# Kernel tuning notes

Hardware: AMD Instinct MI355X
Metric: run time of the kernel (lower is better)

The kernel has to match this reference:

```python
import jax, jax.numpy as jnp
import numpy as np

TREE_DEPTH = 6
IN_F, OUT_F = 1024, 1024
BATCH = 2048
N_LEAVES = 2 ** TREE_DEPTH
N_NODES = N_LEAVES - 1


def _tree_routes(depth):
    """Static routing table: for each leaf, the decision-node index visited at
    each depth and whether the leaf takes the sigmoid (1) or 1-sigmoid (0) branch.
    Mirrors the torch traversal: node = 2*node + 1 + bit; bits of leaf id LSB-first."""
    n_leaves = 2 ** depth
    idx = np.zeros((n_leaves, depth), dtype=np.int32)
    pos = np.zeros((n_leaves, depth), dtype=bool)
    for l in range(n_leaves):
        node, index = 0, l
        for d in range(depth):
            idx[l, d] = node
            pos[l, d] = (index % 2 == 0)
            node = node * 2 + 1 + index % 2
            index >>= 1
    return idx, pos

ROUTE_IDX, ROUTE_POS = _tree_routes(TREE_DEPTH)


def setup_inputs() -> dict:
    key = jax.random.key(0)
    kx, kwd, kwl = jax.random.split(key, 3)
    scale = 0.02  # keep sigmoid/softmax logits in a sane range
    x = jax.random.normal(kx, (BATCH, IN_F), dtype=jnp.float32)
    Wd = jax.random.normal(kwd, (N_NODES, IN_F), dtype=jnp.float32) * scale
    bd = jnp.zeros((N_NODES,), dtype=jnp.float32)
    Wl = jax.random.normal(kwl, (N_LEAVES, OUT_F, IN_F), dtype=jnp.float32) * scale
    bl = jnp.zeros((N_LEAVES, OUT_F), dtype=jnp.float32)
    return {"x": x, "Wd": Wd, "bd": bd, "Wl": Wl, "bl": bl}


def reference(x, Wd, bd, Wl, bl):
    # All decision node probabilities in one GEMM: [B, n_nodes]
    dprob = jax.nn.sigmoid(x @ Wd.T + bd)
    # Gather per-leaf path probs [B, L, depth] and take path product -> routing [B, L]
    path = dprob[:, ROUTE_IDX]                      # [B, L, D]
    path = jnp.where(ROUTE_POS, path, 1.0 - path)
    routing = jnp.prod(path, axis=-1)               # [B, L]
    # All leaf experts in one batched GEMM: [B, L, out], softmax over out (torch dim=1)
    leaf_logits = jnp.einsum('bi,loi->blo', x, Wl) + bl
    leaves = jax.nn.softmax(leaf_logits, axis=-1)
    # Routing-weighted sum over leaves
    return jnp.einsum('bl,blo->bo', routing, leaves)
```

## Files before the change

### kernel.cpp

```cpp
#include <hip/hip_runtime.h>
#include <hip/hip_bf16.h>

#define BATCH 2048
#define KD 1024
#define ND 1024
#define NLEAF 64
#define BM 256
#define BN 256

typedef __attribute__((ext_vector_type(8))) short bf16x8;
typedef __attribute__((ext_vector_type(4))) float f32x4;
typedef __attribute__((ext_vector_type(8))) _Float16 f16x8;

#define WLB_OFF 0ULL
#define XB_OFF  134217728ULL
#define RT_OFF  138412032ULL
#define LG_OFF  138936320ULL

__device__ __forceinline__ unsigned short f2bf(float f) {
  unsigned int u = __float_as_uint(f);
  u += 0x7fffu + ((u >> 16) & 1u);
  return (unsigned short)(u >> 16);
}

__device__ __forceinline__ void gload_lds16(const void* g, void* l) {
  __builtin_amdgcn_global_load_lds(
      (const __attribute__((address_space(1))) unsigned int*)g,
      (__attribute__((address_space(3))) unsigned int*)l, 16, 0, 0);
}

__global__ void __launch_bounds__(256) convert_kernel(
    const float* __restrict__ Wl, const float* __restrict__ x,
    unsigned short* __restrict__ wlb, unsigned short* __restrict__ xb) {
  const long long WL4 = 16777216LL;
  const long long X4  = 524288LL;
  long long i = (long long)blockIdx.x * 256 + threadIdx.x;
  const long long stride = (long long)gridDim.x * 256;
  for (; i < WL4 + X4; i += stride) {
    float4 v;
    if (i < WL4) v = ((const float4*)Wl)[i];
    else         v = ((const float4*)x)[i - WL4];
    ushort4 o;
    o.x = f2bf(v.x); o.y = f2bf(v.y); o.z = f2bf(v.z); o.w = f2bf(v.w);
    if (i < WL4) ((ushort4*)wlb)[i] = o;
    else         ((ushort4*)xb)[i - WL4] = o;
  }
}

__global__ void __launch_bounds__(256) routing_kernel(
    const float* __restrict__ x, const float* __restrict__ Wd,
    const float* __restrict__ bd, float* __restrict__ rt) {
  __shared__ float xs[4][KD];
  __shared__ float sdp[4][64];
  const int tid = threadIdx.x;
  const int b0 = blockIdx.x * 4;
  const float4* xsrc = (const float4*)(x + (size_t)b0 * KD);
  float4* xdst = (float4*)&xs[0][0];
  for (int i = tid; i < KD; i += 256) xdst[i] = xsrc[i];
  __syncthreads();
  const int wv = tid >> 6, ln = tid & 63;
  const int b = b0 + wv;
  if (ln < 63) {
    const float4* wrow = (const float4*)(Wd + (size_t)ln * KD);
    const float4* xr = (const float4*)&xs[wv][0];
    float4 a = {0.f, 0.f, 0.f, 0.f};
    for (int k = 0; k < KD / 4; ++k) {
      float4 w = wrow[k], xv = xr[k];
      a.x += w.x * xv.x; a.y += w.y * xv.y; a.z += w.z * xv.z; a.w += w.w * xv.w;
    }
    float z = a.x + a.y + a.z + a.w + bd[ln];
    sdp[wv][ln] = 1.f / (1.f + __expf(-z));
  }
  __syncthreads();
  float prod = 1.f;
  int node = 0, index = ln;
  for (int d = 0; d < 6; ++d) {
    float pv = sdp[wv][node];
    prod *= (index & 1) ? (1.f - pv) : pv;
    node = node * 2 + 1 + (index & 1);
    index >>= 1;
  }
  rt[(size_t)b * NLEAF + ln] = prod;
}

#define GBODY(CURA, CURB, NXTA, NXTB, S, VMASM, DOREAD)                      \
  {                                                                          \
    if ((S) + 3 < 32) STAGE((S) + 3);                                        \
    asm volatile(VMASM ::: "memory");                                        \
    asm volatile("s_waitcnt lgkmcnt(0)" ::: "memory");                       \
    __builtin_amdgcn_sched_barrier(0);                                       \
    asm volatile("s_barrier" ::: "memory");                                  \
    __builtin_amdgcn_s_setprio(1);                                           \
    if (DOREAD) {                                                            \
      const char* nbuf = smem + (((S) + 1) & 3) * 32768;                     \
      _Pragma("unroll")                                                      \
      for (int mi = 0; mi < 8; ++mi)                                         \
        NXTA[mi] = *(const bf16x8*)(nbuf + offA[mi]);                        \
      _Pragma("unroll")                                                      \
      for (int ni = 0; ni < 4; ++ni)                                         \
        NXTB[ni] = *(const bf16x8*)(nbuf + 16384 + offB[ni]);                \
    }                                                                        \
    _Pragma("unroll")                                                        \
    for (int mi = 0; mi < 8; ++mi)                                           \
      _Pragma("unroll")                                                      \
      for (int ni = 0; ni < 4; ++ni)                                         \
        acc[mi][ni] = __builtin_amdgcn_mfma_f32_16x16x32_bf16(               \
            CURA[mi], CURB[ni], acc[mi][ni], 0, 0, 0);                       \
    if (DOREAD) {                                                            \
      _Pragma("unroll")                                                      \
      for (int r = 0; r < 12; ++r) {                                         \
        __builtin_amdgcn_sched_group_barrier(0x100, 1, 0);    \
        __builtin_amdgcn_sched_group_barrier(0x008, 2, 0);    \
      }                                                                      \
      __builtin_amdgcn_sched_group_barrier(0x008, 8, 0);      \
    }                                                                        \
    __builtin_amdgcn_s_setprio(0);                                           \
    __builtin_amdgcn_sched_barrier(0);                                       \
  }

__global__ void __launch_bounds__(512, 2) gemm_kernel(
    const unsigned short* __restrict__ A, const unsigned short* __restrict__ B,
    const float* __restrict__ blg, _Float16* __restrict__ C, int ntile) {
  extern __shared__ char smem[];
  const int tid = threadIdx.x;
  const int w = tid >> 6, ln = tid & 63;
  const int wm = w >> 2, wn = w & 3;
  const int g = ln >> 4, r16 = ln & 15;
  const int bid = blockIdx.x;
  const int j = bid >> 3;
  const int bm = (j & 7) * BM;
  const int bn = (((j >> 3) << 3) + (bid & 7)) * BN;
  const long long ldc = (long long)ntile * 256;

  const int rS = tid >> 2;
  const int cS = tid & 3;
  const int csrc = cS ^ ((rS >> 1) & 3);
  const unsigned short* ga0 = A + (size_t)(bm + rS) * KD + csrc * 8;
  const unsigned short* ga1 = ga0 + (size_t)128 * KD;
  const unsigned short* gb0 = B + (size_t)(bn + rS) * KD + csrc * 8;
  const unsigned short* gb1 = gb0 + (size_t)128 * KD;
  const int ldsw = w * 1024;

  auto STAGE = [&](int t) {
    char* base = smem + (t & 3) * 32768;
    const size_t ko = (size_t)t * 32;
    gload_lds16(ga0 + ko, base + ldsw);
    gload_lds16(ga1 + ko, base + 8192 + ldsw);
    gload_lds16(gb0 + ko, base + 16384 + ldsw);
    gload_lds16(gb1 + ko, base + 24576 + ldsw);
  };

  int offA[8], offB[4];
#pragma unroll
  for (int mi = 0; mi < 8; ++mi) {
    const int row = wm * 128 + mi * 16 + r16;
    offA[mi] = row * 64 + (g ^ ((row >> 1) & 3)) * 16;
  }
#pragma unroll
  for (int ni = 0; ni < 4; ++ni) {
    const int row = wn * 64 + ni * 16 + r16;
    offB[ni] = row * 64 + (g ^ ((row >> 1) & 3)) * 16;
  }

  f32x4 acc[8][4];
#pragma unroll
  for (int mi = 0; mi < 8; ++mi)
#pragma unroll
    for (int ni = 0; ni < 4; ++ni) acc[mi][ni] = (f32x4){0.f, 0.f, 0.f, 0.f};

  bf16x8 aE[8], bE[4], aO[8], bO[4];

  STAGE(0); STAGE(1); STAGE(2);
  asm volatile("s_waitcnt vmcnt(8)" ::: "memory");
  asm volatile("s_barrier" ::: "memory");
  {
    const char* nbuf = smem;
#pragma unroll
    for (int mi = 0; mi < 8; ++mi) aE[mi] = *(const bf16x8*)(nbuf + offA[mi]);
#pragma unroll
    for (int ni = 0; ni < 4; ++ni) bE[ni] = *(const bf16x8*)(nbuf + 16384 + offB[ni]);
  }

  for (int u = 0; u < 14; ++u) {
    GBODY(aE, bE, aO, bO, 2 * u,     "s_waitcnt vmcnt(8)", 1);
    GBODY(aO, bO, aE, bE, 2 * u + 1, "s_waitcnt vmcnt(8)", 1);
  }
  GBODY(aE, bE, aO, bO, 28, "s_waitcnt vmcnt(8)", 1);
  GBODY(aO, bO, aE, bE, 29, "s_waitcnt vmcnt(4)", 1);
  GBODY(aE, bE, aO, bO, 30, "s_waitcnt vmcnt(0)", 1);
  GBODY(aO, bO, aE, bE, 31, "s_waitcnt vmcnt(0)", 0);

  const int lf = bn >> 10;
  float blv[4];
#pragma unroll
  for (int ni = 0; ni < 4; ++ni)
    blv[ni] = blg[(size_t)lf * ND + (bn & 1023) + wn * 64 + ni * 16 + r16];
#pragma unroll
  for (int mi = 0; mi < 8; ++mi)
#pragma unroll
    for (int q = 0; q < 4; ++q) {
      const long long grow = bm + wm * 128 + mi * 16 + g * 4 + q;
#pragma unroll
      for (int ni = 0; ni < 4; ++ni) {
        const int gcol = bn + wn * 64 + ni * 16 + r16;
        C[grow * ldc + gcol] = (_Float16)(acc[mi][ni][q] + blv[ni]);
      }
    }
}

__global__ void __launch_bounds__(256) smax_kernel(
    const _Float16* __restrict__ Cg, const float* __restrict__ rt,
    float* __restrict__ out, int lpg, int l0, int first) {
  const int tid = threadIdx.x;
  const int wv = tid >> 6, ln = tid & 63;
  const int b = blockIdx.x * 4 + wv;
  const long long ldc = (long long)lpg * ND;
  const _Float16* base = Cg + (size_t)b * ldc + ln * 8;
  const float rtv = (ln < lpg) ? rt[(size_t)b * NLEAF + l0 + ln] : 0.f;

  float oacc[16];
#pragma unroll
  for (int k = 0; k < 16; ++k) oacc[k] = 0.f;

  for (int jj = 0; jj < lpg; ++jj) {
    const f16x8 h0 = *(const f16x8*)(base + jj * ND);
    const f16x8 h1 = *(const f16x8*)(base + jj * ND + 512);
    float e[16], s = 0.f;
#pragma unroll
    for (int k = 0; k < 8; ++k) { e[k] = __expf((float)h0[k]); s += e[k]; }
#pragma unroll
    for (int k = 0; k < 8; ++k) { e[8 + k] = __expf((float)h1[k]); s += e[8 + k]; }
#pragma unroll
    for (int off = 1; off < 64; off <<= 1) s += __shfl_xor(s, off);
    const float coef = __shfl(rtv, jj) / s;
#pragma unroll
    for (int k = 0; k < 16; ++k) oacc[k] += coef * e[k];
  }

  float* o0 = out + (size_t)b * ND + ln * 8;
  if (first) {
    *(float4*)o0         = (float4){oacc[0], oacc[1], oacc[2], oacc[3]};
    *(float4*)(o0 + 4)   = (float4){oacc[4], oacc[5], oacc[6], oacc[7]};
    *(float4*)(o0 + 512) = (float4){oacc[8], oacc[9], oacc[10], oacc[11]};
    *(float4*)(o0 + 516) = (float4){oacc[12], oacc[13], oacc[14], oacc[15]};
  } else {
#pragma unroll
    for (int part = 0; part < 4; ++part) {
      float* p = o0 + (part >> 1) * 512 + (part & 1) * 4;
      float4 v = *(const float4*)p;
      v.x += oacc[part * 4 + 0]; v.y += oacc[part * 4 + 1];
      v.z += oacc[part * 4 + 2]; v.w += oacc[part * 4 + 3];
      *(float4*)p = v;
    }
  }
}

extern "C" void kernel_launch(void* const* d_in, const int* in_sizes, int n_in,
                              void* d_out, int out_size, void* d_ws, size_t ws_size,
                              hipStream_t stream) {
  const float* x  = (const float*)d_in[0];
  const float* Wd = (const float*)d_in[1];
  const float* bd = (const float*)d_in[2];
  const float* Wl = (const float*)d_in[3];
  const float* bl = (const float*)d_in[4];
  float* out = (float*)d_out;
  char* ws = (char*)d_ws;
  unsigned short* wlb = (unsigned short*)(ws + WLB_OFF);
  unsigned short* xb  = (unsigned short*)(ws + XB_OFF);
  float* rt           = (float*)(ws + RT_OFF);
  _Float16* lg        = (_Float16*)(ws + LG_OFF);

  convert_kernel<<<2048, 256, 0, stream>>>(Wl, x, wlb, xb);
  routing_kernel<<<BATCH / 4, 256, 0, stream>>>(x, Wd, bd, rt);
  hipFuncSetAttribute((const void*)gemm_kernel,
                      hipFuncAttributeMaxDynamicSharedMemorySize, 131072);

  const int ngrp = (ws_size >= LG_OFF + (size_t)BATCH * NLEAF * ND * 2) ? 1 : 4;
  const int lpg = NLEAF / ngrp;
  const int ntile = lpg * (ND / BN);
  for (int grp = 0; grp < ngrp; ++grp) {
    gemm_kernel<<<8 * ntile, 512, 131072, stream>>>(
        xb, wlb + (size_t)grp * lpg * ND * KD,
        bl + (size_t)grp * lpg * ND, lg, ntile);
    smax_kernel<<<BATCH / 4, 256, 0, stream>>>(lg, rt, out,
                                               lpg, grp * lpg, grp == 0);
  }
}
```

Before: 498.0 us.

## Shrink GEMM tile to 256x128 with triple-buffered LDS and simpler loop

Halves the N tile of the leaf GEMM to 128 and changes the warp layout to 4x2, giving each wave a 64x64 sub-tile with a 4x4 accumulator. The LDS ring drops from four 32KB stages to three 24KB stages with a prefetch distance of two. The hand-tuned ping-pong register double buffering and sched_group_barrier interleaving are replaced by a plain loop that reads LDS, waits, then runs the MFMAs. The aim is higher occupancy (launch bounds 4) and less LDS use, at the cost of lower arithmetic intensity per tile and losing the overlap of LDS reads with MFMA.

```diff
diff --git a/kernel.cpp b/kernel.cpp
--- a/kernel.cpp
+++ b/kernel.cpp
@@ -6,7 +6,7 @@
 #define ND 1024
 #define NLEAF 64
 #define BM 256
-#define BN 256
+#define BN 128
 
 typedef __attribute__((ext_vector_type(8))) short bf16x8;
 typedef __attribute__((ext_vector_type(4))) float f32x4;
@@ -83,54 +83,19 @@
   rt[(size_t)b * NLEAF + ln] = prod;
 }
 
-#define GBODY(CURA, CURB, NXTA, NXTB, S, VMASM, DOREAD)                      \
-  {                                                                          \
-    if ((S) + 3 < 32) STAGE((S) + 3);                                        \
-    asm volatile(VMASM ::: "memory");                                        \
-    asm volatile("s_waitcnt lgkmcnt(0)" ::: "memory");                       \
-    __builtin_amdgcn_sched_barrier(0);                                       \
-    asm volatile("s_barrier" ::: "memory");                                  \
-    __builtin_amdgcn_s_setprio(1);                                           \
-    if (DOREAD) {                                                            \
-      const char* nbuf = smem + (((S) + 1) & 3) * 32768;                     \
-      _Pragma("unroll")                                                      \
-      for (int mi = 0; mi < 8; ++mi)                                         \
-        NXTA[mi] = *(const bf16x8*)(nbuf + offA[mi]);                        \
-      _Pragma("unroll")                                                      \
-      for (int ni = 0; ni < 4; ++ni)                                         \
-        NXTB[ni] = *(const bf16x8*)(nbuf + 16384 + offB[ni]);                \
-    }                                                                        \
-    _Pragma("unroll")                                                        \
-    for (int mi = 0; mi < 8; ++mi)                                           \
-      _Pragma("unroll")                                                      \
-      for (int ni = 0; ni < 4; ++ni)                                         \
-        acc[mi][ni] = __builtin_amdgcn_mfma_f32_16x16x32_bf16(               \
-            CURA[mi], CURB[ni], acc[mi][ni], 0, 0, 0);                       \
-    if (DOREAD) {                                                            \
-      _Pragma("unroll")                                                      \
-      for (int r = 0; r < 12; ++r) {                                         \
-        __builtin_amdgcn_sched_group_barrier(0x100, 1, 0);    \
-        __builtin_amdgcn_sched_group_barrier(0x008, 2, 0);    \
-      }                                                                      \
-      __builtin_amdgcn_sched_group_barrier(0x008, 8, 0);      \
-    }                                                                        \
-    __builtin_amdgcn_s_setprio(0);                                           \
-    __builtin_amdgcn_sched_barrier(0);                                       \
-  }
-
-__global__ void __launch_bounds__(512, 2) gemm_kernel(
+__global__ void __launch_bounds__(512, 4) gemm_kernel(
     const unsigned short* __restrict__ A, const unsigned short* __restrict__ B,
     const float* __restrict__ blg, _Float16* __restrict__ C, int ntile) {
   extern __shared__ char smem[];
   const int tid = threadIdx.x;
   const int w = tid >> 6, ln = tid & 63;
-  const int wm = w >> 2, wn = w & 3;
+  const int wm = w >> 1, wn = w & 1;
   const int g = ln >> 4, r16 = ln & 15;
   const int bid = blockIdx.x;
   const int j = bid >> 3;
   const int bm = (j & 7) * BM;
   const int bn = (((j >> 3) << 3) + (bid & 7)) * BN;
-  const long long ldc = (long long)ntile * 256;
+  const long long ldc = (long long)ntile * BN;
 
   const int rS = tid >> 2;
   const int cS = tid & 3;
@@ -138,57 +103,61 @@
   const unsigned short* ga0 = A + (size_t)(bm + rS) * KD + csrc * 8;
   const unsigned short* ga1 = ga0 + (size_t)128 * KD;
   const unsigned short* gb0 = B + (size_t)(bn + rS) * KD + csrc * 8;
-  const unsigned short* gb1 = gb0 + (size_t)128 * KD;
   const int ldsw = w * 1024;
 
   auto STAGE = [&](int t) {
-    char* base = smem + (t & 3) * 32768;
+    char* base = smem + (t % 3) * 24576;
     const size_t ko = (size_t)t * 32;
     gload_lds16(ga0 + ko, base + ldsw);
     gload_lds16(ga1 + ko, base + 8192 + ldsw);
     gload_lds16(gb0 + ko, base + 16384 + ldsw);
-    gload_lds16(gb1 + ko, base + 24576 + ldsw);
   };
 
-  int offA[8], offB[4];
-#pragma unroll
-  for (int mi = 0; mi < 8; ++mi) {
-    const int row = wm * 128 + mi * 16 + r16;
+  int offA[4], offB[4];
+#pragma unroll
+  for (int mi = 0; mi < 4; ++mi) {
+    const int row = wm * 64 + mi * 16 + r16;
     offA[mi] = row * 64 + (g ^ ((row >> 1) & 3)) * 16;
   }
 #pragma unroll
   for (int ni = 0; ni < 4; ++ni) {
     const int row = wn * 64 + ni * 16 + r16;
-    offB[ni] = row * 64 + (g ^ ((row >> 1) & 3)) * 16;
-  }
-
-  f32x4 acc[8][4];
-#pragma unroll
-  for (int mi = 0; mi < 8; ++mi)
+    offB[ni] = 16384 + row * 64 + (g ^ ((row >> 1) & 3)) * 16;
+  }
+
+  f32x4 acc[4][4];
+#pragma unroll
+  for (int mi = 0; mi < 4; ++mi)
 #pragma unroll
     for (int ni = 0; ni < 4; ++ni) acc[mi][ni] = (f32x4){0.f, 0.f, 0.f, 0.f};
 
-  bf16x8 aE[8], bE[4], aO[8], bO[4];
-
-  STAGE(0); STAGE(1); STAGE(2);
-  asm volatile("s_waitcnt vmcnt(8)" ::: "memory");
+  STAGE(0); STAGE(1);
+  asm volatile("s_waitcnt vmcnt(3)" ::: "memory");
   asm volatile("s_barrier" ::: "memory");
-  {
-    const char* nbuf = smem;
-#pragma unroll
-    for (int mi = 0; mi < 8; ++mi) aE[mi] = *(const bf16x8*)(nbuf + offA[mi]);
-#pragma unroll
-    for (int ni = 0; ni < 4; ++ni) bE[ni] = *(const bf16x8*)(nbuf + 16384 + offB[ni]);
-  }
-
-  for (int u = 0; u < 14; ++u) {
-    GBODY(aE, bE, aO, bO, 2 * u,     "s_waitcnt vmcnt(8)", 1);
-    GBODY(aO, bO, aE, bE, 2 * u + 1, "s_waitcnt vmcnt(8)", 1);
-  }
-  GBODY(aE, bE, aO, bO, 28, "s_waitcnt vmcnt(8)", 1);
-  GBODY(aO, bO, aE, bE, 29, "s_waitcnt vmcnt(4)", 1);
-  GBODY(aE, bE, aO, bO, 30, "s_waitcnt vmcnt(0)", 1);
-  GBODY(aO, bO, aE, bE, 31, "s_waitcnt vmcnt(0)", 0);
+
+  for (int t = 0; t < 32; ++t) {
+    const char* buf = smem + (t % 3) * 24576;
+    bf16x8 af[4], bf[4];
+#pragma unroll
+    for (int mi = 0; mi < 4; ++mi) af[mi] = *(const bf16x8*)(buf + offA[mi]);
+#pragma unroll
+    for (int ni = 0; ni < 4; ++ni) bf[ni] = *(const bf16x8*)(buf + offB[ni]);
+    asm volatile("s_waitcnt lgkmcnt(0)" ::: "memory");
+    __builtin_amdgcn_sched_barrier(0);
+    if (t + 2 < 32) STAGE(t + 2);
+    if (t < 30) asm volatile("s_waitcnt vmcnt(3)" ::: "memory");
+    else        asm volatile("s_waitcnt vmcnt(0)" ::: "memory");
+    asm volatile("s_barrier" ::: "memory");
+    __builtin_amdgcn_s_setprio(1);
+#pragma unroll
+    for (int mi = 0; mi < 4; ++mi)
+#pragma unroll
+      for (int ni = 0; ni < 4; ++ni)
+        acc[mi][ni] = __builtin_amdgcn_mfma_f32_16x16x32_bf16(
+            af[mi], bf[ni], acc[mi][ni], 0, 0, 0);
+    __builtin_amdgcn_s_setprio(0);
+    __builtin_amdgcn_sched_barrier(0);
+  }
 
   const int lf = bn >> 10;
   float blv[4];
@@ -196,10 +165,10 @@
   for (int ni = 0; ni < 4; ++ni)
     blv[ni] = blg[(size_t)lf * ND + (bn & 1023) + wn * 64 + ni * 16 + r16];
 #pragma unroll
-  for (int mi = 0; mi < 8; ++mi)
+  for (int mi = 0; mi < 4; ++mi)
 #pragma unroll
     for (int q = 0; q < 4; ++q) {
-      const long long grow = bm + wm * 128 + mi * 16 + g * 4 + q;
+      const long long grow = bm + wm * 64 + mi * 16 + g * 4 + q;
 #pragma unroll
       for (int ni = 0; ni < 4; ++ni) {
         const int gcol = bn + wn * 64 + ni * 16 + r16;
@@ -273,13 +242,13 @@
   convert_kernel<<<2048, 256, 0, stream>>>(Wl, x, wlb, xb);
   routing_kernel<<<BATCH / 4, 256, 0, stream>>>(x, Wd, bd, rt);
   hipFuncSetAttribute((const void*)gemm_kernel,
-                      hipFuncAttributeMaxDynamicSharedMemorySize, 131072);
+                      hipFuncAttributeMaxDynamicSharedMemorySize, 73728);
 
   const int ngrp = (ws_size >= LG_OFF + (size_t)BATCH * NLEAF * ND * 2) ? 1 : 4;
   const int lpg = NLEAF / ngrp;
   const int ntile = lpg * (ND / BN);
   for (int grp = 0; grp < ngrp; ++grp) {
-    gemm_kernel<<<8 * ntile, 512, 131072, stream>>>(
+    gemm_kernel<<<8 * ntile, 512, 73728, stream>>>(
         xb, wlb + (size_t)grp * lpg * ND * KD,
         bl + (size_t)grp * lpg * ND, lg, ntile);
     smax_kernel<<<BATCH / 4, 256, 0, stream>>>(lg, rt, out,
```

Result: no change. 505.0 us (+1.4%).
